# Performance work log

Hardware: AMD Instinct MI355X
Metric: run time of the kernel (lower is better)

## Reference

```python
import jax, jax.numpy as jnp
import numpy as np

B, T, C = 4, 2048, 1024
H = 16
HS = C // H

def setup_inputs() -> dict:
    key = jax.random.key(0)
    ks = jax.random.split(key, 5)
    s = 0.02
    return {
        "x": jax.random.normal(ks[0], (B, T, C), dtype=jnp.float32),
        "c_attn_w": jax.random.normal(ks[1], (C, 3 * C), dtype=jnp.float32) * s,
        "c_attn_b": jax.random.normal(ks[2], (3 * C,), dtype=jnp.float32) * s,
        "c_proj_w": jax.random.normal(ks[3], (C, C), dtype=jnp.float32) * s,
        "c_proj_b": jax.random.normal(ks[4], (C,), dtype=jnp.float32) * s,
    }

def reference(x, c_attn_w, c_attn_b, c_proj_w, c_proj_b):
    b, t, c = x.shape
    qkv = x @ c_attn_w + c_attn_b                       # (B,T,3C)
    q, k, v = jnp.split(qkv, 3, axis=2)
    # (B,T,C) -> (B,H,T,hs)
    q = q.reshape(b, t, H, HS).transpose(0, 2, 1, 3)
    k = k.reshape(b, t, H, HS).transpose(0, 2, 1, 3)
    v = v.reshape(b, t, H, HS).transpose(0, 2, 1, 3)
    scale = 1.0 / np.sqrt(HS).astype(np.float32)
    attn = jnp.einsum("bhqd,bhkd->bhqk", q, k) * scale  # (B,H,T,T)
    causal = jnp.tril(jnp.ones((t, t), dtype=bool))
    attn = jnp.where(causal[None, None, :, :], attn, -jnp.inf)
    attn = jax.nn.softmax(attn, axis=-1)
    y = jnp.einsum("bhqk,bhkd->bhqd", attn, v)          # (B,H,T,hs)
    y = y.transpose(0, 2, 1, 3).reshape(b, t, c)        # (B,T,C)
    return y @ c_proj_w + c_proj_b
```

## Files before the change

### kernel.cpp

```cpp
#include <hip/hip_runtime.h>

typedef __attribute__((ext_vector_type(8))) _Float16 h8;
typedef __attribute__((ext_vector_type(4))) _Float16 h4;
typedef __attribute__((ext_vector_type(4))) float f4;
typedef __attribute__((ext_vector_type(16))) float f16x;
typedef __attribute__((ext_vector_type(4))) unsigned u4;

#define MFMA16(a,b,c) __builtin_amdgcn_mfma_f32_16x16x32_f16(a,b,c,0,0,0)
#define MFMA32(a,b,c) __builtin_amdgcn_mfma_f32_32x32x16_f16(a,b,c,0,0,0)

__device__ inline void gload16(const void* g, void* l) {
    __builtin_amdgcn_global_load_lds(
        (const __attribute__((address_space(1))) void*)g,
        (__attribute__((address_space(3))) void*)l, 16, 0, 0);
}

__device__ inline float swap_half(float x) { return __shfl_xor(x, 32, 64); }

__global__ __launch_bounds__(256) void k_f32_to_f16(const float* __restrict__ in,
                                                    _Float16* __restrict__ out, int n4) {
    int i = blockIdx.x * 256 + threadIdx.x;
    if (i < n4) {
        float4 v = ((const float4*)in)[i];
        h4 h;
        h[0] = (_Float16)v.x; h[1] = (_Float16)v.y;
        h[2] = (_Float16)v.z; h[3] = (_Float16)v.w;
        ((h4*)out)[i] = h;
    }
}

__global__ __launch_bounds__(256) void k_transpose_f16(const float* __restrict__ W,
                                                       _Float16* __restrict__ Wt,
                                                       int K, int N) {
    __shared__ float tile[64 * 68];
    const int k0 = blockIdx.x * 64, n0 = blockIdx.y * 64;
    const int t = threadIdx.x;
    const int tr = t >> 4;
    const int tc = t & 15;
#pragma unroll
    for (int i = 0; i < 4; ++i) {
        int r = tr + i * 16;
        float4 v = *(const float4*)(W + (size_t)(k0 + r) * N + n0 + tc * 4);
        *(float4*)(&tile[r * 68 + tc * 4]) = v;
    }
    __syncthreads();
#pragma unroll
    for (int i = 0; i < 4; ++i) {
        int nl = tr + i * 16;
        h4 hv;
#pragma unroll
        for (int j = 0; j < 4; ++j)
            hv[j] = (_Float16)tile[(tc * 4 + j) * 68 + nl];
        *(h4*)(Wt + (size_t)(n0 + nl) * K + k0 + tc * 4) = hv;
    }
}

template <int BN, int MODE>
__global__ __launch_bounds__(512, 2) void k_gemm2(const _Float16* __restrict__ A,
                                                  const _Float16* __restrict__ Bt,
                                                  const float* __restrict__ bias,
                                                  _Float16* __restrict__ oQ,
                                                  _Float16* __restrict__ oK,
                                                  _Float16* __restrict__ oV,
                                                  float* __restrict__ oF,
                                                  int K, int N, int nbn) {
    constexpr int NF = BN / 64;
    __shared__ _Float16 As[2][256 * 64];
    __shared__ _Float16 Bs[2][BN * 64];
    const int nwg = gridDim.x;
    const int q8 = nwg >> 3;
    const int wg = (blockIdx.x & 7) * q8 + (blockIdx.x >> 3);
    const int bm = (wg / nbn) * 256, bn = (wg % nbn) * BN;
    const int tid = threadIdx.x, lane = tid & 63, wv = tid >> 6;
    const int wm = wv >> 2, wn = wv & 3;
    const int l15 = lane & 15, l4 = lane >> 4;
    const int sr8 = lane >> 3;
    const int sseg = ((lane & 7) ^ sr8) * 8;
    const _Float16* Ag = A + (size_t)(bm + wv * 8 + sr8) * K + sseg;
    const _Float16* Bg = Bt + (size_t)(bn + wv * 8 + sr8) * K + sseg;
    f4 acc[8][NF] = {};

    const int NT = K >> 6;

#pragma unroll
    for (int j = 0; j < 4; ++j) gload16(Ag + (size_t)j * 64 * K, &As[0][(j * 64 + wv * 8) * 64]);
#pragma unroll
    for (int j = 0; j < NF; ++j) gload16(Bg + (size_t)j * 64 * K, &Bs[0][(j * 64 + wv * 8) * 64]);
    asm volatile("s_waitcnt vmcnt(0)" ::: "memory");
    __builtin_amdgcn_s_barrier();

    for (int tau = 0; tau < NT; ++tau) {
        const int s = tau & 1;
        const bool pre = (tau + 1 < NT);
        const size_t ko = (size_t)(tau + 1) << 6;

        h8 bf[NF][2];
#pragma unroll
        for (int nf = 0; nf < NF; ++nf)
#pragma unroll
            for (int ks = 0; ks < 2; ++ks) {
                const int row = wn * (BN / 4) + nf * 16 + l15;
                const int seg = (ks * 4 + l4) ^ (l15 & 7);
                bf[nf][ks] = *(const h8*)(&Bs[s][row * 64 + seg * 8]);
            }

#pragma unroll
        for (int q = 0; q < 4; ++q) {
            h8 af[2][2];
#pragma unroll
            for (int mi = 0; mi < 2; ++mi)
#pragma unroll
                for (int ks = 0; ks < 2; ++ks) {
                    const int row = wm * 128 + (2 * q + mi) * 16 + l15;
                    const int seg = (ks * 4 + l4) ^ (l15 & 7);
                    af[mi][ks] = *(const h8*)(&As[s][row * 64 + seg * 8]);
                }
            if (pre) {
                if (q == 0) {
                    gload16(Ag + ko, &As[s ^ 1][(wv * 8) * 64]);
                    gload16(Ag + (size_t)64 * K + ko, &As[s ^ 1][(64 + wv * 8) * 64]);
                } else if (q == 1) {
                    gload16(Ag + (size_t)128 * K + ko, &As[s ^ 1][(128 + wv * 8) * 64]);
                    gload16(Ag + (size_t)192 * K + ko, &As[s ^ 1][(192 + wv * 8) * 64]);
                } else if (q == 2) {
#pragma unroll
                    for (int j = 0; j < NF; ++j)
                        gload16(Bg + (size_t)j * 64 * K + ko, &Bs[s ^ 1][(j * 64 + wv * 8) * 64]);
                } else {
                    asm volatile("s_waitcnt vmcnt(0)" ::: "memory");
                }
            }
            __builtin_amdgcn_s_barrier();
            __builtin_amdgcn_s_setprio(1);
#pragma unroll
            for (int mi = 0; mi < 2; ++mi)
#pragma unroll
                for (int nf = 0; nf < NF; ++nf)
#pragma unroll
                    for (int ks = 0; ks < 2; ++ks)
                        acc[2 * q + mi][nf] = MFMA16(af[mi][ks], bf[nf][ks], acc[2 * q + mi][nf]);
            __builtin_amdgcn_s_setprio(0);
            __builtin_amdgcn_s_barrier();
        }
    }

#pragma unroll
    for (int mf = 0; mf < 8; ++mf) {
#pragma unroll
        for (int nf = 0; nf < NF; ++nf) {
            const int col = bn + wn * (BN / 4) + nf * 16 + l15;
            const float bv = bias[col];
            const int rb = bm + wm * 128 + mf * 16 + l4 * 4;
            if (MODE == 0) {
                const int which = col >> 10;
                const int hh = (col & 1023) >> 6, dd = col & 63;
                if (which == 2) {
                    const int b = rb >> 11, tq = rb & 2047;
                    h4 pv;
#pragma unroll
                    for (int i = 0; i < 4; ++i) pv[i] = (_Float16)(acc[mf][nf][i] + bv);
                    *(h4*)(oV + ((size_t)(b * 16 + hh) * 64 + dd) * 2048 + tq) = pv;
                } else {
                    _Float16* dst = which == 0 ? oQ : oK;
                    const float scl = which == 0 ? 0.18033688011112042f : 1.0f;
#pragma unroll
                    for (int i = 0; i < 4; ++i) {
                        const int row = rb + i;
                        const int b = row >> 11, tq = row & 2047;
                        dst[(((size_t)b * 16 + hh) * 2048 + tq) * 64 + dd] =
                            (_Float16)((acc[mf][nf][i] + bv) * scl);
                    }
                }
            } else {
#pragma unroll
                for (int i = 0; i < 4; ++i)
                    oF[(size_t)(rb + i) * N + col] = acc[mf][nf][i] + bv;
            }
        }
    }
}

#define SWZI(row, cb) ((((row) << 7) + ((cb) ^ ((((row) & 7) << 4)))) >> 1)

__global__ __launch_bounds__(256) void k_attn(const _Float16* __restrict__ Qh,
                                              const _Float16* __restrict__ Kh,
                                              const _Float16* __restrict__ Vt,
                                              _Float16* __restrict__ Yh) {
    __shared__ _Float16 lds[8192];
    const int bid = blockIdx.x;
    const int bh = bid & 63;
    const int qt = 15 - (bid >> 6);
    const int tid = threadIdx.x, w = tid >> 6;
    const int l31 = tid & 31, hi = (tid >> 5) & 1;
    const int h16 = hi * 16, h4o = hi * 4;
    const size_t base = (size_t)bh * 2048 * 64;

    const int qabs = qt * 128 + w * 32 + l31;
    h8 qf[4];
#pragma unroll
    for (int dk = 0; dk < 4; ++dk)
        qf[dk] = *(const h8*)(Qh + base + (size_t)qabs * 64 + dk * 16 + hi * 8);

    f16x O0 = {}, O1 = {};
    float m = -1e30f, l = 0.f;

    const int sr = tid >> 3;
    const int sc8 = (tid & 7) * 8;
    const int scb = (tid & 7) * 16;
    const int kbb = 2 * qt + 1;
    const int kbw = 2 * qt + (w >> 1);

    {
#pragma unroll
        for (int j = 0; j < 2; ++j) {
            int row = j * 32 + sr;
            h8 kv = *(const h8*)(Kh + base + (size_t)row * 64 + sc8);
            h8 vv = *(const h8*)(Vt + base + (size_t)row * 2048 + sc8);
            *(h8*)(&lds[SWZI(row, scb)]) = kv;
            *(h8*)(&lds[4096 + SWZI(row, scb)]) = vv;
        }
    }
    __syncthreads();

    for (int kb = 0; kb <= kbb; ++kb) {
        const bool pre = (kb < kbb);
        h8 kn[2], vn[2];
        if (pre) {
#pragma unroll
            for (int j = 0; j < 2; ++j) {
                int row = j * 32 + sr;
                kn[j] = *(const h8*)(Kh + base + (size_t)((kb + 1) * 64 + row) * 64 + sc8);
                vn[j] = *(const h8*)(Vt + base + (size_t)row * 2048 + (kb + 1) * 64 + sc8);
            }
        }

        if (kb <= kbw) {
            f16x S0 = {}, S1 = {};
            __builtin_amdgcn_s_setprio(1);
#pragma unroll
            for (int dk = 0; dk < 4; ++dk) {
                h8 kf0 = *(const h8*)(&lds[SWZI(l31, dk * 32 + h16)]);
                h8 kf1 = *(const h8*)(&lds[SWZI(32 + l31, dk * 32 + h16)]);
                S0 = MFMA32(kf0, qf[dk], S0);
                S1 = MFMA32(kf1, qf[dk], S1);
            }
            __builtin_amdgcn_s_setprio(0);

            if (kb == kbw) {
#pragma unroll
                for (int r = 0; r < 16; ++r) {
                    int key = kb * 64 + (r & 3) + 8 * (r >> 2) + h4o;
                    if (key > qabs) S0[r] = -1e30f;
                    if (key + 32 > qabs) S1[r] = -1e30f;
                }
            }

            float tr[16];
#pragma unroll
            for (int r = 0; r < 16; ++r) tr[r] = fmaxf(S0[r], S1[r]);
#pragma unroll
            for (int st = 8; st >= 1; st >>= 1)
#pragma unroll
                for (int r = 0; r < st; ++r) tr[r] = fmaxf(tr[r], tr[r + st]);
            float pm = fmaxf(tr[0], swap_half(tr[0]));
            if (!__all(pm - m <= 8.f)) {
                float mnew = fmaxf(m, pm);
                float scl = __builtin_amdgcn_exp2f(m - mnew);
                m = mnew;
                l *= scl;
#pragma unroll
                for (int r = 0; r < 16; ++r) { O0[r] *= scl; O1[r] *= scl; }
            }
#pragma unroll
            for (int r = 0; r < 16; ++r) {
                S0[r] = __builtin_amdgcn_exp2f(S0[r] - m);
                S1[r] = __builtin_amdgcn_exp2f(S1[r] - m);
            }
#pragma unroll
            for (int r = 0; r < 16; ++r) tr[r] = S0[r] + S1[r];
#pragma unroll
            for (int st = 8; st >= 1; st >>= 1)
#pragma unroll
                for (int r = 0; r < st; ++r) tr[r] += tr[r + st];
            l += tr[0] + swap_half(tr[0]);

            h8 pb[4];
#pragma unroll
            for (int kk = 0; kk < 4; ++kk) {
                const int bb = (kk & 1) * 8;
                unsigned W0, W1, W2, W3;
                if (kk < 2) {
                    W0 = __builtin_bit_cast(unsigned, __builtin_amdgcn_cvt_pkrtz(S0[bb + 0], S0[bb + 1]));
                    W1 = __builtin_bit_cast(unsigned, __builtin_amdgcn_cvt_pkrtz(S0[bb + 2], S0[bb + 3]));
                    W2 = __builtin_bit_cast(unsigned, __builtin_amdgcn_cvt_pkrtz(S0[bb + 4], S0[bb + 5]));
                    W3 = __builtin_bit_cast(unsigned, __builtin_amdgcn_cvt_pkrtz(S0[bb + 6], S0[bb + 7]));
                } else {
                    W0 = __builtin_bit_cast(unsigned, __builtin_amdgcn_cvt_pkrtz(S1[bb + 0], S1[bb + 1]));
                    W1 = __builtin_bit_cast(unsigned, __builtin_amdgcn_cvt_pkrtz(S1[bb + 2], S1[bb + 3]));
                    W2 = __builtin_bit_cast(unsigned, __builtin_amdgcn_cvt_pkrtz(S1[bb + 4], S1[bb + 5]));
                    W3 = __builtin_bit_cast(unsigned, __builtin_amdgcn_cvt_pkrtz(S1[bb + 6], S1[bb + 7]));
                }
                unsigned E0 = (unsigned)__shfl_xor((int)(hi ? W0 : W2), 32, 64);
                unsigned E1 = (unsigned)__shfl_xor((int)(hi ? W1 : W3), 32, 64);
                u4 wvv;
                wvv[0] = hi ? E0 : W0;
                wvv[1] = hi ? E1 : W1;
                wvv[2] = hi ? W2 : E0;
                wvv[3] = hi ? W3 : E1;
                pb[kk] = __builtin_bit_cast(h8, wvv);
            }

            __builtin_amdgcn_s_setprio(1);
#pragma unroll
            for (int kk = 0; kk < 4; ++kk) {
                h8 vf0 = *(const h8*)(&lds[4096 + SWZI(l31, kk * 32 + h16)]);
                h8 vf1 = *(const h8*)(&lds[4096 + SWZI(32 + l31, kk * 32 + h16)]);
                O0 = MFMA32(vf0, pb[kk], O0);
                O1 = MFMA32(vf1, pb[kk], O1);
            }
            __builtin_amdgcn_s_setprio(0);
        }

        __syncthreads();
        if (pre) {
#pragma unroll
            for (int j = 0; j < 2; ++j) {
                int row = j * 32 + sr;
                *(h8*)(&lds[SWZI(row, scb)]) = kn[j];
                *(h8*)(&lds[4096 + SWZI(row, scb)]) = vn[j];
            }
            __syncthreads();
        }
    }

    __syncthreads();

    {
        float inv = 1.0f / l;
        const int R = w * 32 + l31;
#pragma unroll
        for (int rr = 0; rr < 4; ++rr) {
            h4 a, b;
#pragma unroll
            for (int q = 0; q < 4; ++q) {
                a[q] = (_Float16)(O0[rr * 4 + q] * inv);
                b[q] = (_Float16)(O1[rr * 4 + q] * inv);
            }
            *(h4*)(&lds[SWZI(R, rr * 16 + hi * 8)]) = a;
            *(h4*)(&lds[SWZI(R, 64 + rr * 16 + hi * 8)]) = b;
        }
    }
    __syncthreads();
    {
        const int b = bh >> 4, head = bh & 15;
        const int row = tid >> 1;
#pragma unroll
        for (int i = 0; i < 4; ++i) {
            int seg = (tid & 1) * 4 + i;
            h8 v = *(const h8*)(&lds[SWZI(row, seg * 16)]);
            *(h8*)(Yh + ((size_t)(b * 2048 + qt * 128 + row)) * 1024 + head * 64 + seg * 8) = v;
        }
    }
}

extern "C" void kernel_launch(void* const* d_in, const int* in_sizes, int n_in,
                              void* d_out, int out_size, void* d_ws, size_t ws_size,
                              hipStream_t stream) {
    const float* x  = (const float*)d_in[0];
    const float* Wa = (const float*)d_in[1];
    const float* ba = (const float*)d_in[2];
    const float* Wp = (const float*)d_in[3];
    const float* bp = (const float*)d_in[4];
    float* out = (float*)d_out;

    _Float16* ws = (_Float16*)d_ws;
    const size_t SZ_X = (size_t)8192 * 1024;
    const size_t SZ_WA = (size_t)3072 * 1024;
    const size_t SZ_WP = (size_t)1024 * 1024;
    const size_t SZ_H = (size_t)64 * 2048 * 64;
    _Float16* xh  = ws;
    _Float16* WaT = xh + SZ_X;
    _Float16* WpT = WaT + SZ_WA;
    _Float16* Qh  = WpT + SZ_WP;
    _Float16* Kh  = Qh + SZ_H;
    _Float16* Vth = Kh + SZ_H;
    _Float16* Yh  = Vth + SZ_H;

    k_f32_to_f16<<<8192, 256, 0, stream>>>(x, xh, (int)(SZ_X / 4));
    k_transpose_f16<<<dim3(16, 48), 256, 0, stream>>>(Wa, WaT, 1024, 3072);
    k_transpose_f16<<<dim3(16, 16), 256, 0, stream>>>(Wp, WpT, 1024, 1024);
    k_gemm2<192, 0><<<512, 512, 0, stream>>>(xh, WaT, ba, Qh, Kh, Vth, nullptr,
                                             1024, 3072, 16);
    k_attn<<<1024, 256, 0, stream>>>(Qh, Kh, Vth, Yh);
    k_gemm2<128, 1><<<256, 512, 0, stream>>>(Yh, WpT, bp, nullptr, nullptr, nullptr,
                                             out, 1024, 1024, 8);
}
```

Before: 181.9 us.

## Triple-buffer GEMM LDS pipeline and fix BN to 128 for both projections

Replaces the double-buffered GEMM with a three-stage LDS ring that prefetches two k-tiles ahead, waiting with vmcnt(6) instead of draining all loads each iteration. The QKV projection moves from 192-wide N tiles on 512 blocks to 128-wide tiles on 768 blocks. The goal is to hide global-load latency better and balance work across CUs. In exchange, LDS use per block rises to 144 KB (three 32 KB A stages plus three 16 KB B stages), which may limit blocks per CU and cut occupancy below the launch bound of 2.

```diff
diff --git a/kernel.cpp b/kernel.cpp
--- a/kernel.cpp
+++ b/kernel.cpp
@@ -55,8 +55,8 @@
     }
 }
 
-template <int BN, int MODE>
-__global__ __launch_bounds__(512, 2) void k_gemm2(const _Float16* __restrict__ A,
+template <int MODE>
+__global__ __launch_bounds__(512, 2) void k_gemm3(const _Float16* __restrict__ A,
                                                   const _Float16* __restrict__ Bt,
                                                   const float* __restrict__ bias,
                                                   _Float16* __restrict__ oQ,
@@ -64,13 +64,12 @@
                                                   _Float16* __restrict__ oV,
                                                   float* __restrict__ oF,
                                                   int K, int N, int nbn) {
-    constexpr int NF = BN / 64;
-    __shared__ _Float16 As[2][256 * 64];
-    __shared__ _Float16 Bs[2][BN * 64];
+    __shared__ _Float16 As[3][256 * 64];
+    __shared__ _Float16 Bs[3][128 * 64];
     const int nwg = gridDim.x;
     const int q8 = nwg >> 3;
     const int wg = (blockIdx.x & 7) * q8 + (blockIdx.x >> 3);
-    const int bm = (wg / nbn) * 256, bn = (wg % nbn) * BN;
+    const int bm = (wg / nbn) * 256, bn = (wg % nbn) * 128;
     const int tid = threadIdx.x, lane = tid & 63, wv = tid >> 6;
     const int wm = wv >> 2, wn = wv & 3;
     const int l15 = lane & 15, l4 = lane >> 4;
@@ -78,30 +77,42 @@
     const int sseg = ((lane & 7) ^ sr8) * 8;
     const _Float16* Ag = A + (size_t)(bm + wv * 8 + sr8) * K + sseg;
     const _Float16* Bg = Bt + (size_t)(bn + wv * 8 + sr8) * K + sseg;
-    f4 acc[8][NF] = {};
+    f4 acc[8][2] = {};
 
     const int NT = K >> 6;
 
-#pragma unroll
-    for (int j = 0; j < 4; ++j) gload16(Ag + (size_t)j * 64 * K, &As[0][(j * 64 + wv * 8) * 64]);
-#pragma unroll
-    for (int j = 0; j < NF; ++j) gload16(Bg + (size_t)j * 64 * K, &Bs[0][(j * 64 + wv * 8) * 64]);
-    asm volatile("s_waitcnt vmcnt(0)" ::: "memory");
+    auto stageA01 = [&](size_t ko, int s) {
+        gload16(Ag + ko, &As[s][(wv * 8) * 64]);
+        gload16(Ag + (size_t)64 * K + ko, &As[s][(64 + wv * 8) * 64]);
+    };
+    auto stageA23 = [&](size_t ko, int s) {
+        gload16(Ag + (size_t)128 * K + ko, &As[s][(128 + wv * 8) * 64]);
+        gload16(Ag + (size_t)192 * K + ko, &As[s][(192 + wv * 8) * 64]);
+    };
+    auto stageB = [&](size_t ko, int s) {
+        gload16(Bg + ko, &Bs[s][(wv * 8) * 64]);
+        gload16(Bg + (size_t)64 * K + ko, &Bs[s][(64 + wv * 8) * 64]);
+    };
+
+    stageA01(0, 0); stageA23(0, 0); stageB(0, 0);
+    stageA01(64, 1); stageA23(64, 1); stageB(64, 1);
+    asm volatile("s_waitcnt vmcnt(6)" ::: "memory");
     __builtin_amdgcn_s_barrier();
 
+    int cs = 0;
     for (int tau = 0; tau < NT; ++tau) {
-        const int s = tau & 1;
-        const bool pre = (tau + 1 < NT);
-        const size_t ko = (size_t)(tau + 1) << 6;
-
-        h8 bf[NF][2];
-#pragma unroll
-        for (int nf = 0; nf < NF; ++nf)
+        const int s2 = cs + 2 >= 3 ? cs - 1 : cs + 2;
+        const bool pre2 = (tau + 2 < NT);
+        const size_t ko2 = (size_t)(tau + 2) << 6;
+
+        h8 bf[2][2];
+#pragma unroll
+        for (int nf = 0; nf < 2; ++nf)
 #pragma unroll
             for (int ks = 0; ks < 2; ++ks) {
-                const int row = wn * (BN / 4) + nf * 16 + l15;
+                const int row = wn * 32 + nf * 16 + l15;
                 const int seg = (ks * 4 + l4) ^ (l15 & 7);
-                bf[nf][ks] = *(const h8*)(&Bs[s][row * 64 + seg * 8]);
+                bf[nf][ks] = *(const h8*)(&Bs[cs][row * 64 + seg * 8]);
             }
 
 #pragma unroll
@@ -113,42 +124,35 @@
                 for (int ks = 0; ks < 2; ++ks) {
                     const int row = wm * 128 + (2 * q + mi) * 16 + l15;
                     const int seg = (ks * 4 + l4) ^ (l15 & 7);
-                    af[mi][ks] = *(const h8*)(&As[s][row * 64 + seg * 8]);
+                    af[mi][ks] = *(const h8*)(&As[cs][row * 64 + seg * 8]);
                 }
-            if (pre) {
-                if (q == 0) {
-                    gload16(Ag + ko, &As[s ^ 1][(wv * 8) * 64]);
-                    gload16(Ag + (size_t)64 * K + ko, &As[s ^ 1][(64 + wv * 8) * 64]);
-                } else if (q == 1) {
-                    gload16(Ag + (size_t)128 * K + ko, &As[s ^ 1][(128 + wv * 8) * 64]);
-                    gload16(Ag + (size_t)192 * K + ko, &As[s ^ 1][(192 + wv * 8) * 64]);
-                } else if (q == 2) {
-#pragma unroll
-                    for (int j = 0; j < NF; ++j)
-                        gload16(Bg + (size_t)j * 64 * K + ko, &Bs[s ^ 1][(j * 64 + wv * 8) * 64]);
-                } else {
-                    asm volatile("s_waitcnt vmcnt(0)" ::: "memory");
-                }
+            if (q == 0) { if (pre2) stageA01(ko2, s2); }
+            else if (q == 1) { if (pre2) stageA23(ko2, s2); }
+            else if (q == 2) { if (pre2) stageB(ko2, s2); }
+            else {
+                if (pre2)              asm volatile("s_waitcnt vmcnt(6)" ::: "memory");
+                else if (tau + 1 < NT) asm volatile("s_waitcnt vmcnt(0)" ::: "memory");
             }
             __builtin_amdgcn_s_barrier();
             __builtin_amdgcn_s_setprio(1);
 #pragma unroll
             for (int mi = 0; mi < 2; ++mi)
 #pragma unroll
-                for (int nf = 0; nf < NF; ++nf)
+                for (int nf = 0; nf < 2; ++nf)
 #pragma unroll
                     for (int ks = 0; ks < 2; ++ks)
                         acc[2 * q + mi][nf] = MFMA16(af[mi][ks], bf[nf][ks], acc[2 * q + mi][nf]);
             __builtin_amdgcn_s_setprio(0);
             __builtin_amdgcn_s_barrier();
         }
+        cs = cs + 1 == 3 ? 0 : cs + 1;
     }
 
 #pragma unroll
     for (int mf = 0; mf < 8; ++mf) {
 #pragma unroll
-        for (int nf = 0; nf < NF; ++nf) {
-            const int col = bn + wn * (BN / 4) + nf * 16 + l15;
+        for (int nf = 0; nf < 2; ++nf) {
+            const int col = bn + wn * 32 + nf * 16 + l15;
             const float bv = bias[col];
             const int rb = bm + wm * 128 + mf * 16 + l4 * 4;
             if (MODE == 0) {
@@ -389,9 +393,9 @@
     k_f32_to_f16<<<8192, 256, 0, stream>>>(x, xh, (int)(SZ_X / 4));
     k_transpose_f16<<<dim3(16, 48), 256, 0, stream>>>(Wa, WaT, 1024, 3072);
     k_transpose_f16<<<dim3(16, 16), 256, 0, stream>>>(Wp, WpT, 1024, 1024);
-    k_gemm2<192, 0><<<512, 512, 0, stream>>>(xh, WaT, ba, Qh, Kh, Vth, nullptr,
-                                             1024, 3072, 16);
+    k_gemm3<0><<<768, 512, 0, stream>>>(xh, WaT, ba, Qh, Kh, Vth, nullptr,
+                                        1024, 3072, 24);
     k_attn<<<1024, 256, 0, stream>>>(Qh, Kh, Vth, Yh);
-    k_gemm2<128, 1><<<256, 512, 0, stream>>>(Yh, WpT, bp, nullptr, nullptr, nullptr,
-                                             out, 1024, 1024, 8);
-}
+    k_gemm3<1><<<256, 512, 0, stream>>>(Yh, WpT, bp, nullptr, nullptr, nullptr,
+                                        out, 1024, 1024, 8);
+}
```

Result: slower. 201.6 us (+10.9%).

## Rewrite QKV GEMM with 256x256 tiles and 4-stage K=32 pipeline

Applied to the files above, without the earlier changes.

Splits the templated GEMM into a dedicated QKV kernel and a projection kernel. The QKV kernel now uses 256x256 output tiles (384 workgroups instead of 512) and a four-deep ring of K=32 LDS buffers. Each stage's A and B loads are staggered across the two MFMA halves with graded vmcnt waits, so more global loads stay in flight while the matrix units run. The projection GEMM is unchanged apart from specialization. The trade-offs are a larger per-thread accumulator array, which adds register pressure, and fewer workgroups than the 256 CUs can evenly absorb (1.5 waves).

```diff
diff --git a/kernel.cpp b/kernel.cpp
--- a/kernel.cpp
+++ b/kernel.cpp
@@ -55,22 +55,133 @@
     }
 }
 
-template <int BN, int MODE>
-__global__ __launch_bounds__(512, 2) void k_gemm2(const _Float16* __restrict__ A,
+__global__ __launch_bounds__(512, 2) void k_gemmA(const _Float16* __restrict__ A,
                                                   const _Float16* __restrict__ Bt,
                                                   const float* __restrict__ bias,
                                                   _Float16* __restrict__ oQ,
                                                   _Float16* __restrict__ oK,
                                                   _Float16* __restrict__ oV,
-                                                  float* __restrict__ oF,
-                                                  int K, int N, int nbn) {
-    constexpr int NF = BN / 64;
-    __shared__ _Float16 As[2][256 * 64];
-    __shared__ _Float16 Bs[2][BN * 64];
+                                                  int K, int nbn) {
+    __shared__ _Float16 As[4][256 * 32];
+    __shared__ _Float16 Bs[4][256 * 32];
     const int nwg = gridDim.x;
     const int q8 = nwg >> 3;
     const int wg = (blockIdx.x & 7) * q8 + (blockIdx.x >> 3);
-    const int bm = (wg / nbn) * 256, bn = (wg % nbn) * BN;
+    const int bm = (wg / nbn) * 256, bn = (wg % nbn) * 256;
+    const int tid = threadIdx.x, lane = tid & 63, wv = tid >> 6;
+    const int wm = wv >> 2, wn = wv & 3;
+    const int l15 = lane & 15, l4 = lane >> 4;
+    const int rseg8 = (l4 ^ ((l15 >> 1) & 3)) * 8;
+
+    const int srow = tid >> 2;
+    const int sseg = ((tid & 3) ^ ((tid >> 3) & 3));
+    const _Float16* Ag = A + (size_t)(bm + srow) * K + sseg * 8;
+    const _Float16* Bg = Bt + (size_t)(bn + srow) * K + sseg * 8;
+
+    f4 acc[8][4] = {};
+    const int NSUB = K >> 5;
+
+    auto STAGE_A = [&](int t3, int s) {
+        const size_t ko = (size_t)t3 * 32;
+        gload16(Ag + ko, &As[s][wv * 512]);
+        gload16(Ag + (size_t)128 * K + ko, &As[s][4096 + wv * 512]);
+    };
+    auto STAGE_B = [&](int t3, int s) {
+        const size_t ko = (size_t)t3 * 32;
+        gload16(Bg + ko, &Bs[s][wv * 512]);
+        gload16(Bg + (size_t)128 * K + ko, &Bs[s][4096 + wv * 512]);
+    };
+
+    STAGE_A(0, 0); STAGE_B(0, 0);
+    STAGE_A(1, 1); STAGE_B(1, 1);
+    STAGE_A(2, 2); STAGE_B(2, 2);
+    asm volatile("s_waitcnt vmcnt(8)" ::: "memory");
+    __builtin_amdgcn_s_barrier();
+
+    for (int t = 0; t < NSUB; ++t) {
+        const int s = t & 3, s3 = (t + 3) & 3;
+        const bool st = (t + 3 < NSUB);
+        const _Float16* Ac = As[s];
+        const _Float16* Bc = Bs[s];
+
+        h8 af[4], bf[4];
+#pragma unroll
+        for (int mf = 0; mf < 4; ++mf)
+            af[mf] = *(const h8*)(&Ac[(wm * 128 + mf * 16 + l15) * 32 + rseg8]);
+#pragma unroll
+        for (int nf = 0; nf < 4; ++nf)
+            bf[nf] = *(const h8*)(&Bc[(wn * 64 + nf * 16 + l15) * 32 + rseg8]);
+        if (st) STAGE_A(t + 3, s3);
+        __builtin_amdgcn_s_barrier();
+        __builtin_amdgcn_s_setprio(1);
+#pragma unroll
+        for (int mf = 0; mf < 4; ++mf)
+#pragma unroll
+            for (int nf = 0; nf < 4; ++nf)
+                acc[mf][nf] = MFMA16(af[mf], bf[nf], acc[mf][nf]);
+        __builtin_amdgcn_s_setprio(0);
+        __builtin_amdgcn_s_barrier();
+
+        h8 ag[4];
+#pragma unroll
+        for (int mf = 0; mf < 4; ++mf)
+            ag[mf] = *(const h8*)(&Ac[(wm * 128 + (mf + 4) * 16 + l15) * 32 + rseg8]);
+        if (st) STAGE_B(t + 3, s3);
+        if (t + 3 < NSUB)      asm volatile("s_waitcnt vmcnt(8)" ::: "memory");
+        else if (t + 2 < NSUB) asm volatile("s_waitcnt vmcnt(4)" ::: "memory");
+        else if (t + 1 < NSUB) asm volatile("s_waitcnt vmcnt(0)" ::: "memory");
+        __builtin_amdgcn_s_barrier();
+        __builtin_amdgcn_s_setprio(1);
+#pragma unroll
+        for (int mf = 0; mf < 4; ++mf)
+#pragma unroll
+            for (int nf = 0; nf < 4; ++nf)
+                acc[mf + 4][nf] = MFMA16(ag[mf], bf[nf], acc[mf + 4][nf]);
+        __builtin_amdgcn_s_setprio(0);
+        __builtin_amdgcn_s_barrier();
+    }
+
+#pragma unroll
+    for (int mf = 0; mf < 8; ++mf) {
+#pragma unroll
+        for (int nf = 0; nf < 4; ++nf) {
+            const int col = bn + wn * 64 + nf * 16 + l15;
+            const float bv = bias[col];
+            const int rb = bm + wm * 128 + mf * 16 + l4 * 4;
+            const int which = col >> 10;
+            const int hh = (col & 1023) >> 6, dd = col & 63;
+            if (which == 2) {
+                const int b = rb >> 11, tq = rb & 2047;
+                h4 pv;
+#pragma unroll
+                for (int i = 0; i < 4; ++i) pv[i] = (_Float16)(acc[mf][nf][i] + bv);
+                *(h4*)(oV + ((size_t)(b * 16 + hh) * 64 + dd) * 2048 + tq) = pv;
+            } else {
+                _Float16* dst = which == 0 ? oQ : oK;
+                const float scl = which == 0 ? 0.18033688011112042f : 1.0f;
+#pragma unroll
+                for (int i = 0; i < 4; ++i) {
+                    const int row = rb + i;
+                    const int b = row >> 11, tq = row & 2047;
+                    dst[(((size_t)b * 16 + hh) * 2048 + tq) * 64 + dd] =
+                        (_Float16)((acc[mf][nf][i] + bv) * scl);
+                }
+            }
+        }
+    }
+}
+
+__global__ __launch_bounds__(512, 2) void k_gemmP(const _Float16* __restrict__ A,
+                                                  const _Float16* __restrict__ Bt,
+                                                  const float* __restrict__ bias,
+                                                  float* __restrict__ oF,
+                                                  int K, int N, int nbn) {
+    __shared__ _Float16 As[2][256 * 64];
+    __shared__ _Float16 Bs[2][128 * 64];
+    const int nwg = gridDim.x;
+    const int q8 = nwg >> 3;
+    const int wg = (blockIdx.x & 7) * q8 + (blockIdx.x >> 3);
+    const int bm = (wg / nbn) * 256, bn = (wg % nbn) * 128;
     const int tid = threadIdx.x, lane = tid & 63, wv = tid >> 6;
     const int wm = wv >> 2, wn = wv & 3;
     const int l15 = lane & 15, l4 = lane >> 4;
@@ -78,14 +189,13 @@
     const int sseg = ((lane & 7) ^ sr8) * 8;
     const _Float16* Ag = A + (size_t)(bm + wv * 8 + sr8) * K + sseg;
     const _Float16* Bg = Bt + (size_t)(bn + wv * 8 + sr8) * K + sseg;
-    f4 acc[8][NF] = {};
+    f4 acc[8][2] = {};
 
     const int NT = K >> 6;
-
 #pragma unroll
     for (int j = 0; j < 4; ++j) gload16(Ag + (size_t)j * 64 * K, &As[0][(j * 64 + wv * 8) * 64]);
 #pragma unroll
-    for (int j = 0; j < NF; ++j) gload16(Bg + (size_t)j * 64 * K, &Bs[0][(j * 64 + wv * 8) * 64]);
+    for (int j = 0; j < 2; ++j) gload16(Bg + (size_t)j * 64 * K, &Bs[0][(j * 64 + wv * 8) * 64]);
     asm volatile("s_waitcnt vmcnt(0)" ::: "memory");
     __builtin_amdgcn_s_barrier();
 
@@ -94,12 +204,12 @@
         const bool pre = (tau + 1 < NT);
         const size_t ko = (size_t)(tau + 1) << 6;
 
-        h8 bf[NF][2];
-#pragma unroll
-        for (int nf = 0; nf < NF; ++nf)
+        h8 bf[2][2];
+#pragma unroll
+        for (int nf = 0; nf < 2; ++nf)
 #pragma unroll
             for (int ks = 0; ks < 2; ++ks) {
-                const int row = wn * (BN / 4) + nf * 16 + l15;
+                const int row = wn * 32 + nf * 16 + l15;
                 const int seg = (ks * 4 + l4) ^ (l15 & 7);
                 bf[nf][ks] = *(const h8*)(&Bs[s][row * 64 + seg * 8]);
             }
@@ -124,7 +234,7 @@
                     gload16(Ag + (size_t)192 * K + ko, &As[s ^ 1][(192 + wv * 8) * 64]);
                 } else if (q == 2) {
 #pragma unroll
-                    for (int j = 0; j < NF; ++j)
+                    for (int j = 0; j < 2; ++j)
                         gload16(Bg + (size_t)j * 64 * K + ko, &Bs[s ^ 1][(j * 64 + wv * 8) * 64]);
                 } else {
                     asm volatile("s_waitcnt vmcnt(0)" ::: "memory");
@@ -135,7 +245,7 @@
 #pragma unroll
             for (int mi = 0; mi < 2; ++mi)
 #pragma unroll
-                for (int nf = 0; nf < NF; ++nf)
+                for (int nf = 0; nf < 2; ++nf)
 #pragma unroll
                     for (int ks = 0; ks < 2; ++ks)
                         acc[2 * q + mi][nf] = MFMA16(af[mi][ks], bf[nf][ks], acc[2 * q + mi][nf]);
@@ -145,39 +255,16 @@
     }
 
 #pragma unroll
-    for (int mf = 0; mf < 8; ++mf) {
-#pragma unroll
-        for (int nf = 0; nf < NF; ++nf) {
-            const int col = bn + wn * (BN / 4) + nf * 16 + l15;
+    for (int mf = 0; mf < 8; ++mf)
+#pragma unroll
+        for (int nf = 0; nf < 2; ++nf) {
+            const int col = bn + wn * 32 + nf * 16 + l15;
             const float bv = bias[col];
             const int rb = bm + wm * 128 + mf * 16 + l4 * 4;
-            if (MODE == 0) {
-                const int which = col >> 10;
-                const int hh = (col & 1023) >> 6, dd = col & 63;
-                if (which == 2) {
-                    const int b = rb >> 11, tq = rb & 2047;
-                    h4 pv;
-#pragma unroll
-                    for (int i = 0; i < 4; ++i) pv[i] = (_Float16)(acc[mf][nf][i] + bv);
-                    *(h4*)(oV + ((size_t)(b * 16 + hh) * 64 + dd) * 2048 + tq) = pv;
-                } else {
-                    _Float16* dst = which == 0 ? oQ : oK;
-                    const float scl = which == 0 ? 0.18033688011112042f : 1.0f;
-#pragma unroll
-                    for (int i = 0; i < 4; ++i) {
-                        const int row = rb + i;
-                        const int b = row >> 11, tq = row & 2047;
-                        dst[(((size_t)b * 16 + hh) * 2048 + tq) * 64 + dd] =
-                            (_Float16)((acc[mf][nf][i] + bv) * scl);
-                    }
-                }
-            } else {
-#pragma unroll
-                for (int i = 0; i < 4; ++i)
-                    oF[(size_t)(rb + i) * N + col] = acc[mf][nf][i] + bv;
-            }
-        }
-    }
+#pragma unroll
+            for (int i = 0; i < 4; ++i)
+                oF[(size_t)(rb + i) * N + col] = acc[mf][nf][i] + bv;
+        }
 }
 
 #define SWZI(row, cb) ((((row) << 7) + ((cb) ^ ((((row) & 7) << 4)))) >> 1)
@@ -389,9 +476,7 @@
     k_f32_to_f16<<<8192, 256, 0, stream>>>(x, xh, (int)(SZ_X / 4));
     k_transpose_f16<<<dim3(16, 48), 256, 0, stream>>>(Wa, WaT, 1024, 3072);
     k_transpose_f16<<<dim3(16, 16), 256, 0, stream>>>(Wp, WpT, 1024, 1024);
-    k_gemm2<192, 0><<<512, 512, 0, stream>>>(xh, WaT, ba, Qh, Kh, Vth, nullptr,
-                                             1024, 3072, 16);
+    k_gemmA<<<384, 512, 0, stream>>>(xh, WaT, ba, Qh, Kh, Vth, 1024, 12);
     k_attn<<<1024, 256, 0, stream>>>(Qh, Kh, Vth, Yh);
-    k_gemm2<128, 1><<<256, 512, 0, stream>>>(Yh, WpT, bp, nullptr, nullptr, nullptr,
-                                             out, 1024, 1024, 8);
-}
+    k_gemmP<<<256, 512, 0, stream>>>(Yh, WpT, bp, out, 1024, 1024, 8);
+}
```

Result: slower. 187.7 us (+3.2%).
